# Kernel tuning notes

Hardware: AMD Instinct MI355X
Metric: run time of the kernel (lower is better)

The kernel has to match this reference:

```python
import jax, jax.numpy as jnp
import numpy as np

H = 128  # hidden size


def _gru_scan(xp, w_hh, b_hh):
    # xp: [T, B, 3H] precomputed input projections, PyTorch gate order (r, z, n)
    h0 = jnp.zeros((xp.shape[1], H), xp.dtype)
    def step(h, xt):
        g = h @ w_hh.T + b_hh
        xr, xz, xn = jnp.split(xt, 3, axis=-1)
        hr, hz, hn = jnp.split(g, 3, axis=-1)
        r = jax.nn.sigmoid(xr + hr)
        z = jax.nn.sigmoid(xz + hz)
        n = jnp.tanh(xn + r * hn)
        h = (1.0 - z) * n + z * h
        return h, h
    h_T, ys = jax.lax.scan(step, h0, xp)
    return h_T, ys


def _bidir_layer(x, wi_f, wh_f, bi_f, bh_f, wi_b, wh_b, bi_b, bh_b):
    # x: [T, B, D_in] time-major; returns concat outputs [T, B, 2H] and final hiddens
    h_f, y_f = _gru_scan(x @ wi_f.T + bi_f, wh_f, bh_f)
    h_b, y_b = _gru_scan(x[::-1] @ wi_b.T + bi_b, wh_b, bh_b)
    return jnp.concatenate([y_f, y_b[::-1]], axis=-1), h_f, h_b


def setup_inputs() -> dict:
    key = jax.random.key(0)
    ks = iter(jax.random.split(key, 40))
    scale = 1.0 / np.sqrt(H)
    def p(shape):
        return jax.random.normal(next(ks), shape, jnp.float32) * scale
    inp = {"x": jax.random.normal(next(ks), (512, 512, 4), jnp.float32)}
    for l, din in ((0, 4), (1, 2 * H)):
        for d in ("f", "b"):
            inp[f"w_ih_l{l}{d}"] = p((3 * H, din))
            inp[f"w_hh_l{l}{d}"] = p((3 * H, H))
            inp[f"b_ih_l{l}{d}"] = p((3 * H,))
            inp[f"b_hh_l{l}{d}"] = p((3 * H,))
    inp["fc1_w"] = p((H, 2 * H)); inp["fc1_b"] = p((H,))
    inp["fc2_w"] = p((2, H));     inp["fc2_b"] = p((2,))
    return inp


def reference(x, w_ih_l0f, w_hh_l0f, b_ih_l0f, b_hh_l0f,
              w_ih_l0b, w_hh_l0b, b_ih_l0b, b_hh_l0b,
              w_ih_l1f, w_hh_l1f, b_ih_l1f, b_hh_l1f,
              w_ih_l1b, w_hh_l1b, b_ih_l1b, b_hh_l1b,
              fc1_w, fc1_b, fc2_w, fc2_b):
    xt = jnp.transpose(x, (1, 0, 2))  # [T, B, F] time-major
    y0, _, _ = _bidir_layer(xt, w_ih_l0f, w_hh_l0f, b_ih_l0f, b_hh_l0f,
                            w_ih_l0b, w_hh_l0b, b_ih_l0b, b_hh_l0b)
    # dropout between layers is identity in eval mode
    _, h_f, h_b = _bidir_layer(y0, w_ih_l1f, w_hh_l1f, b_ih_l1f, b_hh_l1f,
                               w_ih_l1b, w_hh_l1b, b_ih_l1b, b_hh_l1b)
    h = jnp.concatenate([h_f, h_b], axis=-1)  # [B, 2H] = last-layer final hiddens, fwd then bwd
    h = jax.nn.relu(h @ fc1_w.T + fc1_b)
    return h @ fc2_w.T + fc2_b  # [B, num_classes]
```

## Files before the change

kernel.cpp:

```cpp
#include <hip/hip_runtime.h>
#include <stdint.h>


#define Tt 512
#define Bb 512
#define THREADS 512

using s16x8 = __attribute__((ext_vector_type(8))) short;
using f32x4 = __attribute__((ext_vector_type(4))) float;

#define MF(a, b, c) __builtin_amdgcn_mfma_f32_16x16x32_bf16((a), (b), (c), 0, 0, 0)

__device__ __forceinline__ unsigned short f2bf(float f) {
    union { float f; unsigned int u; } v; v.f = f;
    unsigned int u = v.u;
    u += 0x7fffu + ((u >> 16) & 1u);
    return (unsigned short)(u >> 16);
}
__device__ __forceinline__ float bf2f(unsigned short h) {
    union { unsigned int u; float f; } v; v.u = ((unsigned int)h) << 16;
    return v.f;
}

__device__ __forceinline__ float fsig(float x) {
    return __builtin_amdgcn_rcpf(1.0f + __expf(-x));
}
__device__ __forceinline__ float ftanh(float x) {
    return 2.0f * __builtin_amdgcn_rcpf(1.0f + __expf(-2.0f * x)) - 1.0f;
}

#define WG_BARRIER() asm volatile("s_waitcnt lgkmcnt(0)\n\ts_barrier" ::: "memory")

__global__ void w_prep(const float* __restrict__ wihf, const float* __restrict__ wihb,
                       const float* __restrict__ bihf, const float* __restrict__ bihb,
                       unsigned short* __restrict__ wcat, float* __restrict__ bcat)
{
    const int n = blockIdx.x;
    const int k = threadIdx.x;
    const float* src = (n < 384) ? &wihf[(size_t)n * 256] : &wihb[(size_t)(n - 384) * 256];
    wcat[(size_t)n * 256 + k] = f2bf(src[k]);
    if (k == 0) bcat[n] = (n < 384) ? bihf[n] : bihb[n - 384];
}

__global__ __launch_bounds__(THREADS) void l1_step(
    const unsigned short* __restrict__ y0,
    const unsigned short* __restrict__ wcat,
    const float* __restrict__ bcat,
    const unsigned short* __restrict__ gx_rd,
    unsigned short* __restrict__ gx_wr,
    const float* __restrict__ whh_f, const float* __restrict__ bhh_f,
    const float* __restrict__ whh_b, const float* __restrict__ bhh_b,
    float* __restrict__ hstate,
    int CT, int kgemm, int nscan, int first)
{
    const int bid  = blockIdx.x;
    const int tid  = threadIdx.x;
    const int wave = tid >> 6;
    const int lane = tid & 63;
    const int lcol = lane & 15;
    const int quad = lane >> 4;

    __shared__ __align__(16) unsigned short lA[128][136];
    __shared__ __align__(16) unsigned short lB[128][136];
    __shared__ __align__(16) unsigned short lds_h[2][16][136];

    if (bid >= nscan) {
        int gb = bid - nscan;
        const int nt = gb % 3;  gb /= 3;
        const int bt = gb & 3;  gb >>= 2;
        const int sl = gb % CT;
        const int dir = gb / CT;
        const int s  = kgemm * CT + sl;
        const int t  = dir ? (511 - s) : s;
        const int bb = bt << 7;

        const unsigned short* Abase = y0 + ((size_t)t * 512 + bb) * 256;
        const unsigned short* Bbase = wcat + ((size_t)dir * 384 + nt * 128) * 256;

        const int r0 = (wave >> 2) * 64;
        const int c0 = (wave & 3) * 32;

        f32x4 acc[4][2];
#pragma unroll
        for (int ti = 0; ti < 4; ++ti)
#pragma unroll
            for (int tj = 0; tj < 2; ++tj) acc[ti][tj] = {0.f, 0.f, 0.f, 0.f};

        const int rstg = tid >> 4;
        const int cstg = (tid & 15) * 8;

#pragma unroll
        for (int kh = 0; kh < 2; ++kh) {
            if (kh) __syncthreads();
#pragma unroll
            for (int it = 0; it < 4; ++it) {
                const int r = it * 32 + rstg;
                *(ulonglong2*)&lA[r][cstg] =
                    *(const ulonglong2*)&Abase[(size_t)r * 256 + kh * 128 + cstg];
                *(ulonglong2*)&lB[r][cstg] =
                    *(const ulonglong2*)&Bbase[(size_t)r * 256 + kh * 128 + cstg];
            }
            __syncthreads();

#pragma unroll
            for (int kk = 0; kk < 4; ++kk) {
                s16x8 af[4], bfv[2];
#pragma unroll
                for (int ti = 0; ti < 4; ++ti)
                    af[ti] = *(const s16x8*)&lA[r0 + ti * 16 + lcol][kk * 32 + quad * 8];
#pragma unroll
                for (int tj = 0; tj < 2; ++tj)
                    bfv[tj] = *(const s16x8*)&lB[c0 + tj * 16 + lcol][kk * 32 + quad * 8];
#pragma unroll
                for (int ti = 0; ti < 4; ++ti)
#pragma unroll
                    for (int tj = 0; tj < 2; ++tj)
                        acc[ti][tj] = MF(af[ti], bfv[tj], acc[ti][tj]);
            }
        }

        float bias[2];
#pragma unroll
        for (int tj = 0; tj < 2; ++tj)
            bias[tj] = bcat[dir * 384 + nt * 128 + c0 + tj * 16 + lcol];

        __syncthreads();

        unsigned short* lC = &lA[0][0];
#pragma unroll
        for (int ti = 0; ti < 4; ++ti)
#pragma unroll
            for (int tj = 0; tj < 2; ++tj) {
                const int col = c0 + tj * 16 + lcol;
#pragma unroll
                for (int i = 0; i < 4; ++i)
                    lC[(size_t)(r0 + ti * 16 + 4 * quad + i) * 136 + col] =
                        f2bf(acc[ti][tj][i] + bias[tj]);
            }
        __syncthreads();

        unsigned short* ob = gx_wr + ((size_t)(dir * CT + sl) * 512 + bb) * 384 + nt * 128;
#pragma unroll
        for (int it = 0; it < 4; ++it) {
            const int r = it * 32 + rstg;
            *(ulonglong2*)&ob[(size_t)r * 384 + cstg] =
                *(const ulonglong2*)&lC[(size_t)r * 136 + cstg];
        }
        return;
    }

    const int dir   = bid >> 5;
    const int chunk = bid & 31;
    const int b0    = chunk * 16;
    const int c     = 16 * wave + lcol;

    const float* whh = dir ? whh_b : whh_f;
    const float* bhh = dir ? bhh_b : bhh_f;

    const float bhr = bhh[c];
    const float bhz = bhh[128 + c];
    const float bhn = bhh[256 + c];

    s16x8 bh[3][4];
#pragma unroll
    for (int p = 0; p < 3; ++p) {
        const int nrow = p * 128 + c;
#pragma unroll
        for (int kk = 0; kk < 4; ++kk) {
            const float* src = &whh[(size_t)nrow * 128 + kk * 32 + quad * 8];
            s16x8 f;
#pragma unroll
            for (int j = 0; j < 8; ++j) f[j] = (short)f2bf(src[j]);
            bh[p][kk] = f;
        }
    }

    const unsigned short* gbase = gx_rd + (size_t)dir * CT * 512 * 384;
    auto loadGX = [&](unsigned short (&G)[12], int sl) {
        const unsigned short* gp = gbase + ((size_t)sl * 512 + b0 + 4 * quad) * 384;
#pragma unroll
        for (int g = 0; g < 3; ++g)
#pragma unroll
            for (int i = 0; i < 4; ++i)
                G[g * 4 + i] = gp[(size_t)i * 384 + g * 128 + c];
    };
    unsigned short G0[12], G1[12];
    loadGX(G0, 0);
    loadGX(G1, 1);

    float hreg[4];
    const int gb2 = tid >> 5;
    const int j0  = (tid & 31) * 4;
    if (first) {
#pragma unroll
        for (int i = 0; i < 4; ++i) hreg[i] = 0.f;
        ushort4 z4; z4.x = 0; z4.y = 0; z4.z = 0; z4.w = 0;
        *(ushort4*)&lds_h[0][gb2][j0] = z4;
    } else {
#pragma unroll
        for (int i = 0; i < 4; ++i)
            hreg[i] = hstate[(size_t)(b0 + 4 * quad + i) * 256 + dir * 128 + c];
        ushort4 hv;
        hv.x = f2bf(hstate[(size_t)(b0 + gb2) * 256 + dir * 128 + j0 + 0]);
        hv.y = f2bf(hstate[(size_t)(b0 + gb2) * 256 + dir * 128 + j0 + 1]);
        hv.z = f2bf(hstate[(size_t)(b0 + gb2) * 256 + dir * 128 + j0 + 2]);
        hv.w = f2bf(hstate[(size_t)(b0 + gb2) * 256 + dir * 128 + j0 + 3]);
        *(ushort4*)&lds_h[0][gb2][j0] = hv;
    }
    __syncthreads();

#define L1C_STEP(S, PAR, G)                                                    \
    do {                                                                       \
        const s16x8 a0 = *(const s16x8*)&lds_h[PAR][lcol][0  + quad * 8];      \
        const s16x8 a1 = *(const s16x8*)&lds_h[PAR][lcol][32 + quad * 8];      \
        const s16x8 a2 = *(const s16x8*)&lds_h[PAR][lcol][64 + quad * 8];      \
        const s16x8 a3 = *(const s16x8*)&lds_h[PAR][lcol][96 + quad * 8];      \
        f32x4 rA = {bhr, bhr, bhr, bhr}, rB = {0.f, 0.f, 0.f, 0.f};            \
        f32x4 zA = {bhz, bhz, bhz, bhz}, zB = {0.f, 0.f, 0.f, 0.f};            \
        f32x4 nA = {bhn, bhn, bhn, bhn}, nB = {0.f, 0.f, 0.f, 0.f};            \
        rA = MF(a0, bh[0][0], rA); zA = MF(a0, bh[1][0], zA);                  \
        nA = MF(a0, bh[2][0], nA);                                             \
        rB = MF(a1, bh[0][1], rB); zB = MF(a1, bh[1][1], zB);                  \
        nB = MF(a1, bh[2][1], nB);                                             \
        rA = MF(a2, bh[0][2], rA); zA = MF(a2, bh[1][2], zA);                  \
        nA = MF(a2, bh[2][2], nA);                                             \
        rB = MF(a3, bh[0][3], rB); zB = MF(a3, bh[1][3], zB);                  \
        nB = MF(a3, bh[2][3], nB);                                             \
        _Pragma("unroll")                                                      \
        for (int i = 0; i < 4; ++i) {                                          \
            const float r = fsig(rA[i] + rB[i] + bf2f(G[i]));                  \
            const float z = fsig(zA[i] + zB[i] + bf2f(G[4 + i]));              \
            const float n = ftanh(bf2f(G[8 + i]) + r * (nA[i] + nB[i]));       \
            hreg[i] = (1.0f - z) * n + z * hreg[i];                            \
            lds_h[PAR ^ 1][4 * quad + i][c] = f2bf(hreg[i]);                   \
        }                                                                      \
        if ((S) < CT - 2) {                                                    \
            loadGX(G, (S) + 2);                                                \
        } else if ((S) == CT - 1) {                                            \
            _Pragma("unroll")                                                  \
            for (int i = 0; i < 4; ++i)                                        \
                hstate[(size_t)(b0 + 4 * quad + i) * 256 + dir * 128 + c] =    \
                    hreg[i];                                                   \
        }                                                                      \
        WG_BARRIER();                                                          \
    } while (0)

    for (int sl = 0; sl < CT; sl += 2) {
        L1C_STEP(sl,     0, G0);
        L1C_STEP(sl + 1, 1, G1);
    }
#undef L1C_STEP
}

__global__ __launch_bounds__(THREADS, 1) void gru_l1(
    const unsigned short* __restrict__ y0,
    const float* __restrict__ wih_f, const float* __restrict__ whh_f,
    const float* __restrict__ bih_f, const float* __restrict__ bhh_f,
    const float* __restrict__ wih_b, const float* __restrict__ whh_b,
    const float* __restrict__ bih_b, const float* __restrict__ bhh_b,
    float* __restrict__ finals)
{
    const int tid  = threadIdx.x;
    const int wave = tid >> 6;
    const int lane = tid & 63;
    const int lcol = lane & 15;
    const int quad = lane >> 4;
    const int dir   = blockIdx.x >> 5;
    const int b0    = (blockIdx.x & 31) * 16;
    const int c     = 16 * wave + lcol;

    const float* wih = dir ? wih_b : wih_f;
    const float* whh = dir ? whh_b : whh_f;
    const float* bih = dir ? bih_b : bih_f;
    const float* bhh = dir ? bhh_b : bhh_f;

    __shared__ __align__(16) unsigned short lds_h[2][16][136];

    const float br  = bih[c]       + bhh[c];
    const float bz  = bih[128 + c] + bhh[128 + c];
    const float bnx = bih[256 + c];
    const float bnh = bhh[256 + c];

    s16x8 bh[3][4];
    s16x8 bx[3][8];
#pragma unroll
    for (int p = 0; p < 3; ++p) {
        const int nrow = p * 128 + c;
#pragma unroll
        for (int kk = 0; kk < 4; ++kk) {
            const float* src = &whh[(size_t)nrow * 128 + kk * 32 + quad * 8];
            s16x8 f;
#pragma unroll
            for (int j = 0; j < 8; ++j) f[j] = (short)f2bf(src[j]);
            bh[p][kk] = f;
        }
#pragma unroll
        for (int kk = 0; kk < 8; ++kk) {
            const float* src = &wih[(size_t)nrow * 256 + kk * 32 + quad * 8];
            s16x8 f;
#pragma unroll
            for (int j = 0; j < 8; ++j) f[j] = (short)f2bf(src[j]);
            bx[p][kk] = f;
        }
    }

    auto loadP = [&](s16x8 (&P)[8], int t) {
        const unsigned short* pb = y0 + ((size_t)t * Bb + b0 + lcol) * 256 + quad * 8;
#pragma unroll
        for (int kk = 0; kk < 8; ++kk) P[kk] = *(const s16x8*)(pb + kk * 32);
    };
    s16x8 P0[8], P1[8];
    loadP(P0, dir ? 511 : 0);
    loadP(P1, dir ? 510 : 1);

    f32x4 accr = {br, br, br, br};
    f32x4 accz = {bz, bz, bz, bz};
    f32x4 accnx = {bnx, bnx, bnx, bnx};
#pragma unroll
    for (int kk = 0; kk < 8; ++kk) {
        accr  = MF(P0[kk], bx[0][kk], accr);
        accz  = MF(P0[kk], bx[1][kk], accz);
        accnx = MF(P0[kk], bx[2][kk], accnx);
    }
    loadP(P0, dir ? 509 : 2);

    float hreg[4] = {0.f, 0.f, 0.f, 0.f};
    for (int idx = tid; idx < 2 * 16 * 136; idx += THREADS)
        ((unsigned short*)lds_h)[idx] = 0;
    __syncthreads();

#define L1_STEP(S, PAR, PN)                                                    \
    do {                                                                       \
        const s16x8 a0 = *(const s16x8*)&lds_h[PAR][lcol][0  + quad * 8];      \
        const s16x8 a1 = *(const s16x8*)&lds_h[PAR][lcol][32 + quad * 8];      \
        const s16x8 a2 = *(const s16x8*)&lds_h[PAR][lcol][64 + quad * 8];      \
        const s16x8 a3 = *(const s16x8*)&lds_h[PAR][lcol][96 + quad * 8];      \
        f32x4 acchn = {bnh, bnh, bnh, bnh};                                    \
        accr = MF(a0, bh[0][0], accr); accz = MF(a0, bh[1][0], accz);          \
        acchn = MF(a0, bh[2][0], acchn);                                       \
        accr = MF(a1, bh[0][1], accr); accz = MF(a1, bh[1][1], accz);          \
        acchn = MF(a1, bh[2][1], acchn);                                       \
        accr = MF(a2, bh[0][2], accr); accz = MF(a2, bh[1][2], accz);          \
        acchn = MF(a2, bh[2][2], acchn);                                       \
        accr = MF(a3, bh[0][3], accr); accz = MF(a3, bh[1][3], accz);          \
        acchn = MF(a3, bh[2][3], acchn);                                       \
        _Pragma("unroll")                                                      \
        for (int i = 0; i < 4; ++i) {                                          \
            const float r = fsig(accr[i]);                                     \
            const float z = fsig(accz[i]);                                     \
            const float n = ftanh(accnx[i] + r * acchn[i]);                    \
            hreg[i] = (1.0f - z) * n + z * hreg[i];                            \
            lds_h[PAR ^ 1][4 * quad + i][c] = f2bf(hreg[i]);                   \
        }                                                                      \
        if ((S) < 511) {                                                       \
            accr = {br, br, br, br}; accz = {bz, bz, bz, bz};                  \
            accnx = {bnx, bnx, bnx, bnx};                                      \
            _Pragma("unroll")                                                  \
            for (int kk = 0; kk < 8; ++kk) {                                   \
                accr  = MF(PN[kk], bx[0][kk], accr);                           \
                accz  = MF(PN[kk], bx[1][kk], accz);                           \
                accnx = MF(PN[kk], bx[2][kk], accnx);                          \
            }                                                                  \
            int sp = (S) + 3; if (sp > 511) sp = 511;                          \
            loadP(PN, dir ? (511 - sp) : sp);                                  \
        } else {                                                               \
            _Pragma("unroll")                                                  \
            for (int i = 0; i < 4; ++i)                                        \
                finals[(size_t)(b0 + 4 * quad + i) * 256 + dir * 128 + c] =    \
                    hreg[i];                                                   \
        }                                                                      \
        WG_BARRIER();                                                          \
    } while (0)

    for (int s = 0; s < Tt; s += 2) {
        L1_STEP(s,     0, P1);
        L1_STEP(s + 1, 1, P0);
    }
#undef L1_STEP
}

__global__ __launch_bounds__(THREADS, 1) void gru_l0(
    const float* __restrict__ x,
    const float* __restrict__ wih_f, const float* __restrict__ whh_f,
    const float* __restrict__ bih_f, const float* __restrict__ bhh_f,
    const float* __restrict__ wih_b, const float* __restrict__ whh_b,
    const float* __restrict__ bih_b, const float* __restrict__ bhh_b,
    unsigned short* __restrict__ y0)
{
    const int tid  = threadIdx.x;
    const int wave = tid >> 6;
    const int lane = tid & 63;
    const int lcol = lane & 15;
    const int quad = lane >> 4;
    const int dir   = blockIdx.x >> 7;
    const int chunk = blockIdx.x & 127;
    const int b0    = chunk * 4;
    const int c     = 16 * wave + lcol;

    const float* wih = dir ? wih_b : wih_f;
    const float* whh = dir ? whh_b : whh_f;
    const float* bih = dir ? bih_b : bih_f;
    const float* bhh = dir ? bhh_b : bhh_f;

    __shared__ __align__(16) unsigned short lds_h[2][16][136];

    const float brs  = bih[c]       + bhh[c];
    const float bzs  = bih[128 + c] + bhh[128 + c];
    const float bnxs = bih[256 + c];
    const float bnh  = bhh[256 + c];

    float wr[4], wz[4], wn[4];
#pragma unroll
    for (int f = 0; f < 4; ++f) {
        wr[f] = wih[(c)       * 4 + f];
        wz[f] = wih[(128 + c) * 4 + f];
        wn[f] = wih[(256 + c) * 4 + f];
    }

    s16x8 bh[3][4];
#pragma unroll
    for (int p = 0; p < 3; ++p) {
        const int nrow = p * 128 + c;
#pragma unroll
        for (int kk = 0; kk < 4; ++kk) {
            const float* src = &whh[(size_t)nrow * 128 + kk * 32 + quad * 8];
            s16x8 f;
#pragma unroll
            for (int j = 0; j < 8; ++j) f[j] = (short)f2bf(src[j]);
            bh[p][kk] = f;
        }
    }

    auto loadX = [&](float4& X, int t) {
        X = *(const float4*)&x[((size_t)(b0 + quad) * Tt + t) * 4];
    };
    float4 X0, X1;
    loadX(X0, dir ? 511 : 0);
    loadX(X1, dir ? 510 : 1);

    float hmine = 0.f;
    for (int idx = tid; idx < 2 * 16 * 136; idx += THREADS)
        ((unsigned short*)lds_h)[idx] = 0;
    __syncthreads();

    const int orow = tid >> 7;
    const int ocol = tid & 127;

#define L0_STEP(S, PAR, XC)                                                    \
    do {                                                                       \
        const int t = dir ? (511 - (S)) : (S);                                 \
        const s16x8 a0 = *(const s16x8*)&lds_h[PAR][lcol][0  + quad * 8];      \
        const s16x8 a1 = *(const s16x8*)&lds_h[PAR][lcol][32 + quad * 8];      \
        const s16x8 a2 = *(const s16x8*)&lds_h[PAR][lcol][64 + quad * 8];      \
        const s16x8 a3 = *(const s16x8*)&lds_h[PAR][lcol][96 + quad * 8];      \
        f32x4 accr  = {brs, brs, brs, brs};                                    \
        f32x4 accz  = {bzs, bzs, bzs, bzs};                                    \
        f32x4 acchn = {bnh, bnh, bnh, bnh};                                    \
        accr = MF(a0, bh[0][0], accr); accz = MF(a0, bh[1][0], accz);          \
        acchn = MF(a0, bh[2][0], acchn);                                       \
        accr = MF(a1, bh[0][1], accr); accz = MF(a1, bh[1][1], accz);          \
        acchn = MF(a1, bh[2][1], acchn);                                       \
        accr = MF(a2, bh[0][2], accr); accz = MF(a2, bh[1][2], accz);          \
        acchn = MF(a2, bh[2][2], acchn);                                       \
        accr = MF(a3, bh[0][3], accr); accz = MF(a3, bh[1][3], accz);          \
        acchn = MF(a3, bh[2][3], acchn);                                       \
           \
        const float xr = XC.x * wr[0] + XC.y * wr[1]                           \
                       + XC.z * wr[2] + XC.w * wr[3];                          \
        const float xz = XC.x * wz[0] + XC.y * wz[1]                           \
                       + XC.z * wz[2] + XC.w * wz[3];                          \
        const float xn = bnxs + XC.x * wn[0] + XC.y * wn[1]                    \
                       + XC.z * wn[2] + XC.w * wn[3];                          \
         \
        float rr0 = __shfl(accr[0], lcol), rr1 = __shfl(accr[1], lcol);        \
        float rr2 = __shfl(accr[2], lcol), rr3 = __shfl(accr[3], lcol);        \
        float zz0 = __shfl(accz[0], lcol), zz1 = __shfl(accz[1], lcol);        \
        float zz2 = __shfl(accz[2], lcol), zz3 = __shfl(accz[3], lcol);        \
        float hh0 = __shfl(acchn[0], lcol), hh1 = __shfl(acchn[1], lcol);      \
        float hh2 = __shfl(acchn[2], lcol), hh3 = __shfl(acchn[3], lcol);      \
        const float pr = quad == 0 ? rr0 : quad == 1 ? rr1 : quad == 2 ? rr2 : rr3; \
        const float pz = quad == 0 ? zz0 : quad == 1 ? zz1 : quad == 2 ? zz2 : zz3; \
        const float ph = quad == 0 ? hh0 : quad == 1 ? hh1 : quad == 2 ? hh2 : hh3; \
        {                                                                      \
            const float r = fsig(pr + xr);                                     \
            const float z = fsig(pz + xz);                                     \
            const float n = ftanh(xn + r * ph);                                \
            hmine = (1.0f - z) * n + z * hmine;                                \
            lds_h[PAR ^ 1][quad][c] = f2bf(hmine);                             \
        }                                                                      \
        if ((S) < 510) {                                                       \
            loadX(XC, dir ? (511 - ((S) + 2)) : ((S) + 2));                    \
        }                                                                      \
        WG_BARRIER();                                                          \
        {                                                                      \
                        \
            y0[((size_t)t * Bb + b0 + orow) * 256 + dir * 128 + ocol] =        \
                lds_h[PAR ^ 1][orow][ocol];                                    \
        }                                                                      \
    } while (0)

    for (int s = 0; s < Tt; s += 2) {
        L0_STEP(s,     0, X0);
        L0_STEP(s + 1, 1, X1);
    }
#undef L0_STEP
}

__global__ __launch_bounds__(128) void fc_head(
    const float* __restrict__ finals,
    const float* __restrict__ fc1w, const float* __restrict__ fc1b,
    const float* __restrict__ fc2w, const float* __restrict__ fc2b,
    float* __restrict__ out)
{
    __shared__ float s_in[256];
    __shared__ float s_h1[128];
    const int b = blockIdx.x, tid = threadIdx.x;
    s_in[tid]       = finals[(size_t)b * 256 + tid];
    s_in[tid + 128] = finals[(size_t)b * 256 + 128 + tid];
    __syncthreads();
    float acc = fc1b[tid];
    const float* wrow = &fc1w[tid * 256];
#pragma unroll 8
    for (int i = 0; i < 256; ++i) acc += s_in[i] * wrow[i];
    s_h1[tid] = fmaxf(acc, 0.0f);
    __syncthreads();
    if (tid < 2) {
        float a = fc2b[tid];
        const float* w2 = &fc2w[tid * 128];
#pragma unroll 8
        for (int i = 0; i < 128; ++i) a += s_h1[i] * w2[i];
        out[b * 2 + tid] = a;
    }
}

extern "C" void kernel_launch(void* const* d_in, const int* in_sizes, int n_in,
                              void* d_out, int out_size, void* d_ws, size_t ws_size,
                              hipStream_t stream) {
    const float* x      = (const float*)d_in[0];
    const float* wih0f  = (const float*)d_in[1];
    const float* whh0f  = (const float*)d_in[2];
    const float* bih0f  = (const float*)d_in[3];
    const float* bhh0f  = (const float*)d_in[4];
    const float* wih0b  = (const float*)d_in[5];
    const float* whh0b  = (const float*)d_in[6];
    const float* bih0b  = (const float*)d_in[7];
    const float* bhh0b  = (const float*)d_in[8];
    const float* wih1f  = (const float*)d_in[9];
    const float* whh1f  = (const float*)d_in[10];
    const float* bih1f  = (const float*)d_in[11];
    const float* bhh1f  = (const float*)d_in[12];
    const float* wih1b  = (const float*)d_in[13];
    const float* whh1b  = (const float*)d_in[14];
    const float* bih1b  = (const float*)d_in[15];
    const float* bhh1b  = (const float*)d_in[16];
    const float* fc1w   = (const float*)d_in[17];
    const float* fc1b   = (const float*)d_in[18];
    const float* fc2w   = (const float*)d_in[19];
    const float* fc2b   = (const float*)d_in[20];

    const size_t Y0SZ = 134217728ull;
    const size_t HSSZ = 524288ull;
    const size_t WCSZ = 393216ull;
    const size_t BCSZ = 3072ull;
    const size_t GX_PER_SL = 786432ull;
    const size_t BASE = Y0SZ + HSSZ + WCSZ + BCSZ;

    unsigned short* y0 = (unsigned short*)d_ws;
    float*  hstate = (float*)((char*)d_ws + Y0SZ);
    unsigned short* wcat = (unsigned short*)((char*)d_ws + Y0SZ + HSSZ);
    float*  bcat   = (float*)((char*)d_ws + Y0SZ + HSSZ + WCSZ);
    unsigned short* gx0 = (unsigned short*)((char*)d_ws + BASE);
    float* out = (float*)d_out;

    const int cts[6] = {128, 64, 32, 16, 8, 4};
    int CT = 0, fused = 0;
    for (int i = 0; i < 6; ++i)
        if (BASE + 2ull * cts[i] * GX_PER_SL <= ws_size) { CT = cts[i]; fused = 1; break; }
    if (!CT)
        for (int i = 0; i < 6; ++i)
            if (BASE + (size_t)cts[i] * GX_PER_SL <= ws_size) { CT = cts[i]; break; }

    if (CT > 0) {
        unsigned short* gxb[2];
        gxb[0] = gx0;
        gxb[1] = fused ? (unsigned short*)((char*)gx0 + (size_t)CT * GX_PER_SL) : gx0;

        w_prep<<<dim3(768), dim3(256), 0, stream>>>(wih1f, wih1b, bih1f, bih1b, wcat, bcat);
        gru_l0<<<dim3(256), dim3(THREADS), 0, stream>>>(
            x, wih0f, whh0f, bih0f, bhh0f, wih0b, whh0b, bih0b, bhh0b, y0);
        const int n = Tt / CT;
        if (fused) {
            l1_step<<<dim3(24 * CT), dim3(THREADS), 0, stream>>>(
                y0, wcat, bcat, gxb[0], gxb[0],
                whh1f, bhh1f, whh1b, bhh1b, hstate, CT, 0, 0, 1);
            for (int k = 0; k < n; ++k) {
                const int ng = (k + 1 < n) ? 24 * CT : 0;
                l1_step<<<dim3(64 + ng), dim3(THREADS), 0, stream>>>(
                    y0, wcat, bcat, gxb[k & 1], gxb[(k + 1) & 1],
                    whh1f, bhh1f, whh1b, bhh1b, hstate, CT, k + 1, 64, (k == 0) ? 1 : 0);
            }
        } else {
            for (int k = 0; k < n; ++k) {
                l1_step<<<dim3(24 * CT), dim3(THREADS), 0, stream>>>(
                    y0, wcat, bcat, gxb[0], gxb[0],
                    whh1f, bhh1f, whh1b, bhh1b, hstate, CT, k, 0, 1);
                l1_step<<<dim3(64), dim3(THREADS), 0, stream>>>(
                    y0, wcat, bcat, gxb[0], gxb[0],
                    whh1f, bhh1f, whh1b, bhh1b, hstate, CT, 0, 64, (k == 0) ? 1 : 0);
            }
        }
        fc_head<<<dim3(Bb), dim3(128), 0, stream>>>(hstate, fc1w, fc1b, fc2w, fc2b, out);
    } else {
        float* finals = (float*)((char*)d_ws + Y0SZ);
        gru_l0<<<dim3(256), dim3(THREADS), 0, stream>>>(
            x, wih0f, whh0f, bih0f, bhh0f, wih0b, whh0b, bih0b, bhh0b, y0);
        gru_l1<<<dim3(64), dim3(THREADS), 0, stream>>>(
            y0, wih1f, whh1f, bih1f, bhh1f, wih1b, whh1b, bih1b, bhh1b, finals);
        fc_head<<<dim3(Bb), dim3(128), 0, stream>>>(finals, fc1w, fc1b, fc2w, fc2b, out);
    }
}
```

Measured before the change: 1.100 ms.

## Spread layer-1 recurrence over 256 blocks with four batch rows each

The layer-1 recurrent scan now uses 128 batch chunks of 4 rows per direction, 256 blocks in total, instead of 32 chunks of 16 rows. It reuses the layer-0 scheme: the MFMA runs on a zero-padded 16-row tile, and each lane picks its row's gate preactivation through shuffles. The aim is to occupy more of the GPU's compute units during the latency-bound sequential scan, so each step takes less time. In exchange, three quarters of the MFMA work is wasted on padding rows, and each block keeps its own copy of W_hh in registers.

```diff
diff --git a/kernel.cpp b/kernel.cpp
--- a/kernel.cpp
+++ b/kernel.cpp
@@ -149,9 +149,9 @@
         return;
     }
 
-    const int dir   = bid >> 5;
-    const int chunk = bid & 31;
-    const int b0    = chunk * 16;
+    const int dir   = bid >> 7;
+    const int chunk = bid & 127;
+    const int b0    = chunk * 4;
     const int c     = 16 * wave + lcol;
 
     const float* whh = dir ? whh_b : whh_f;
@@ -176,36 +176,26 @@
     }
 
     const unsigned short* gbase = gx_rd + (size_t)dir * CT * 512 * 384;
-    auto loadGX = [&](unsigned short (&G)[12], int sl) {
-        const unsigned short* gp = gbase + ((size_t)sl * 512 + b0 + 4 * quad) * 384;
-#pragma unroll
-        for (int g = 0; g < 3; ++g)
-#pragma unroll
-            for (int i = 0; i < 4; ++i)
-                G[g * 4 + i] = gp[(size_t)i * 384 + g * 128 + c];
+    auto loadGX = [&](unsigned short (&G)[3], int sl) {
+        const unsigned short* gp = gbase + ((size_t)sl * 512 + b0 + quad) * 384;
+#pragma unroll
+        for (int g = 0; g < 3; ++g) G[g] = gp[g * 128 + c];
     };
-    unsigned short G0[12], G1[12];
+    unsigned short G0[3], G1[3];
     loadGX(G0, 0);
     loadGX(G1, 1);
 
-    float hreg[4];
-    const int gb2 = tid >> 5;
-    const int j0  = (tid & 31) * 4;
+    float hmine;
+    for (int idx = tid; idx < 2 * 16 * 136; idx += THREADS)
+        ((unsigned short*)lds_h)[idx] = 0;
+    __syncthreads();
+    const int irow = tid >> 7, icol = tid & 127;
     if (first) {
-#pragma unroll
-        for (int i = 0; i < 4; ++i) hreg[i] = 0.f;
-        ushort4 z4; z4.x = 0; z4.y = 0; z4.z = 0; z4.w = 0;
-        *(ushort4*)&lds_h[0][gb2][j0] = z4;
+        hmine = 0.f;
     } else {
-#pragma unroll
-        for (int i = 0; i < 4; ++i)
-            hreg[i] = hstate[(size_t)(b0 + 4 * quad + i) * 256 + dir * 128 + c];
-        ushort4 hv;
-        hv.x = f2bf(hstate[(size_t)(b0 + gb2) * 256 + dir * 128 + j0 + 0]);
-        hv.y = f2bf(hstate[(size_t)(b0 + gb2) * 256 + dir * 128 + j0 + 1]);
-        hv.z = f2bf(hstate[(size_t)(b0 + gb2) * 256 + dir * 128 + j0 + 2]);
-        hv.w = f2bf(hstate[(size_t)(b0 + gb2) * 256 + dir * 128 + j0 + 3]);
-        *(ushort4*)&lds_h[0][gb2][j0] = hv;
+        hmine = hstate[(size_t)(b0 + quad) * 256 + dir * 128 + c];
+        lds_h[0][irow][icol] =
+            f2bf(hstate[(size_t)(b0 + irow) * 256 + dir * 128 + icol]);
     }
     __syncthreads();
 
@@ -215,32 +205,38 @@
         const s16x8 a1 = *(const s16x8*)&lds_h[PAR][lcol][32 + quad * 8];      \
         const s16x8 a2 = *(const s16x8*)&lds_h[PAR][lcol][64 + quad * 8];      \
         const s16x8 a3 = *(const s16x8*)&lds_h[PAR][lcol][96 + quad * 8];      \
-        f32x4 rA = {bhr, bhr, bhr, bhr}, rB = {0.f, 0.f, 0.f, 0.f};            \
-        f32x4 zA = {bhz, bhz, bhz, bhz}, zB = {0.f, 0.f, 0.f, 0.f};            \
-        f32x4 nA = {bhn, bhn, bhn, bhn}, nB = {0.f, 0.f, 0.f, 0.f};            \
-        rA = MF(a0, bh[0][0], rA); zA = MF(a0, bh[1][0], zA);                  \
-        nA = MF(a0, bh[2][0], nA);                                             \
-        rB = MF(a1, bh[0][1], rB); zB = MF(a1, bh[1][1], zB);                  \
-        nB = MF(a1, bh[2][1], nB);                                             \
-        rA = MF(a2, bh[0][2], rA); zA = MF(a2, bh[1][2], zA);                  \
-        nA = MF(a2, bh[2][2], nA);                                             \
-        rB = MF(a3, bh[0][3], rB); zB = MF(a3, bh[1][3], zB);                  \
-        nB = MF(a3, bh[2][3], nB);                                             \
-        _Pragma("unroll")                                                      \
-        for (int i = 0; i < 4; ++i) {                                          \
-            const float r = fsig(rA[i] + rB[i] + bf2f(G[i]));                  \
-            const float z = fsig(zA[i] + zB[i] + bf2f(G[4 + i]));              \
-            const float n = ftanh(bf2f(G[8 + i]) + r * (nA[i] + nB[i]));       \
-            hreg[i] = (1.0f - z) * n + z * hreg[i];                            \
-            lds_h[PAR ^ 1][4 * quad + i][c] = f2bf(hreg[i]);                   \
+        f32x4 accr  = {bhr, bhr, bhr, bhr};                                    \
+        f32x4 accz  = {bhz, bhz, bhz, bhz};                                    \
+        f32x4 acchn = {bhn, bhn, bhn, bhn};                                    \
+        accr = MF(a0, bh[0][0], accr); accz = MF(a0, bh[1][0], accz);          \
+        acchn = MF(a0, bh[2][0], acchn);                                       \
+        accr = MF(a1, bh[0][1], accr); accz = MF(a1, bh[1][1], accz);          \
+        acchn = MF(a1, bh[2][1], acchn);                                       \
+        accr = MF(a2, bh[0][2], accr); accz = MF(a2, bh[1][2], accz);          \
+        acchn = MF(a2, bh[2][2], acchn);                                       \
+        accr = MF(a3, bh[0][3], accr); accz = MF(a3, bh[1][3], accz);          \
+        acchn = MF(a3, bh[2][3], acchn);                                       \
+         \
+        float rr0 = __shfl(accr[0], lcol), rr1 = __shfl(accr[1], lcol);        \
+        float rr2 = __shfl(accr[2], lcol), rr3 = __shfl(accr[3], lcol);        \
+        float zz0 = __shfl(accz[0], lcol), zz1 = __shfl(accz[1], lcol);        \
+        float zz2 = __shfl(accz[2], lcol), zz3 = __shfl(accz[3], lcol);        \
+        float hh0 = __shfl(acchn[0], lcol), hh1 = __shfl(acchn[1], lcol);      \
+        float hh2 = __shfl(acchn[2], lcol), hh3 = __shfl(acchn[3], lcol);      \
+        const float pr = quad == 0 ? rr0 : quad == 1 ? rr1 : quad == 2 ? rr2 : rr3; \
+        const float pz = quad == 0 ? zz0 : quad == 1 ? zz1 : quad == 2 ? zz2 : zz3; \
+        const float ph = quad == 0 ? hh0 : quad == 1 ? hh1 : quad == 2 ? hh2 : hh3; \
+        {                                                                      \
+            const float r = fsig(pr + bf2f(G[0]));                             \
+            const float z = fsig(pz + bf2f(G[1]));                             \
+            const float n = ftanh(bf2f(G[2]) + r * ph);                        \
+            hmine = (1.0f - z) * n + z * hmine;                                \
+            lds_h[PAR ^ 1][quad][c] = f2bf(hmine);                             \
         }                                                                      \
         if ((S) < CT - 2) {                                                    \
             loadGX(G, (S) + 2);                                                \
         } else if ((S) == CT - 1) {                                            \
-            _Pragma("unroll")                                                  \
-            for (int i = 0; i < 4; ++i)                                        \
-                hstate[(size_t)(b0 + 4 * quad + i) * 256 + dir * 128 + c] =    \
-                    hreg[i];                                                   \
+            hstate[(size_t)(b0 + quad) * 256 + dir * 128 + c] = hmine;         \
         }                                                                      \
         WG_BARRIER();                                                          \
     } while (0)
@@ -464,14 +460,12 @@
         acchn = MF(a2, bh[2][2], acchn);                                       \
         accr = MF(a3, bh[0][3], accr); accz = MF(a3, bh[1][3], accz);          \
         acchn = MF(a3, bh[2][3], acchn);                                       \
-           \
         const float xr = XC.x * wr[0] + XC.y * wr[1]                           \
                        + XC.z * wr[2] + XC.w * wr[3];                          \
         const float xz = XC.x * wz[0] + XC.y * wz[1]                           \
                        + XC.z * wz[2] + XC.w * wz[3];                          \
         const float xn = bnxs + XC.x * wn[0] + XC.y * wn[1]                    \
                        + XC.z * wn[2] + XC.w * wn[3];                          \
-         \
         float rr0 = __shfl(accr[0], lcol), rr1 = __shfl(accr[1], lcol);        \
         float rr2 = __shfl(accr[2], lcol), rr3 = __shfl(accr[3], lcol);        \
         float zz0 = __shfl(accz[0], lcol), zz1 = __shfl(accz[1], lcol);        \
@@ -493,7 +487,6 @@
         }                                                                      \
         WG_BARRIER();                                                          \
         {                                                                      \
-                        \
             y0[((size_t)t * Bb + b0 + orow) * 256 + dir * 128 + ocol] =        \
                 lds_h[PAR ^ 1][orow][ocol];                                    \
         }                                                                      \
@@ -595,18 +588,18 @@
                 whh1f, bhh1f, whh1b, bhh1b, hstate, CT, 0, 0, 1);
             for (int k = 0; k < n; ++k) {
                 const int ng = (k + 1 < n) ? 24 * CT : 0;
-                l1_step<<<dim3(64 + ng), dim3(THREADS), 0, stream>>>(
+                l1_step<<<dim3(256 + ng), dim3(THREADS), 0, stream>>>(
                     y0, wcat, bcat, gxb[k & 1], gxb[(k + 1) & 1],
-                    whh1f, bhh1f, whh1b, bhh1b, hstate, CT, k + 1, 64, (k == 0) ? 1 : 0);
+                    whh1f, bhh1f, whh1b, bhh1b, hstate, CT, k + 1, 256, (k == 0) ? 1 : 0);
             }
         } else {
             for (int k = 0; k < n; ++k) {
                 l1_step<<<dim3(24 * CT), dim3(THREADS), 0, stream>>>(
                     y0, wcat, bcat, gxb[0], gxb[0],
                     whh1f, bhh1f, whh1b, bhh1b, hstate, CT, k, 0, 1);
-                l1_step<<<dim3(64), dim3(THREADS), 0, stream>>>(
+                l1_step<<<dim3(256), dim3(THREADS), 0, stream>>>(
                     y0, wcat, bcat, gxb[0], gxb[0],
-                    whh1f, bhh1f, whh1b, bhh1b, hstate, CT, 0, 64, (k == 0) ? 1 : 0);
+                    whh1f, bhh1f, whh1b, bhh1b, hstate, CT, 0, 256, (k == 0) ? 1 : 0);
             }
         }
         fc_head<<<dim3(Bb), dim3(128), 0, stream>>>(hstate, fc1w, fc1b, fc2w, fc2b, out);
```

Result: slower. 1.212 ms (+10.2%).
